# Optimization experiments

Hardware: AMD Instinct MI355X
Metric: run time of the kernel (lower is better)

## Reference

```python
import jax, jax.numpy as jnp
import numpy as np
import math

B, N, K, H = 128, 39, 10, 256
RATIO = 0.8
K1 = math.ceil(RATIO * N)    # 32
K2 = math.ceil(RATIO * K1)   # 26
K3 = math.ceil(RATIO * K2)   # 21


def _edge_conv(x_flat, nb, n, w, b):
    # DynamicEdgeConv: per-graph kNN on features (self included, as torch_cluster.knn),
    # message = relu(Linear([x_i, x_j - x_i])), max aggregation over the K neighbors.
    f = x_flat.shape[-1]
    x = x_flat.reshape(nb, n, f)
    sq = jnp.sum(x * x, axis=-1)                                   # [nb,n]
    d = sq[:, :, None] + sq[:, None, :] - 2.0 * jnp.einsum('bif,bjf->bij', x, x)
    _, idx = jax.lax.top_k(-d, K)                                  # [nb,n,K] nearest
    xj = x[jnp.arange(nb)[:, None, None], idx]                     # [nb,n,K,f]
    xi = x[:, :, None, :]
    msg = jnp.concatenate([jnp.broadcast_to(xi, xj.shape), xj - xi], axis=-1)
    h = jax.nn.relu(msg @ w + b)
    return jnp.max(h, axis=2).reshape(nb * n, -1)


def _gcn_score(x_flat, adj, w, b):
    # GCNConv(in,1) with self-loops + symmetric normalization (SAGPool score layer)
    nb, n, _ = adj.shape
    x = x_flat.reshape(nb, n, -1)
    a = adj + jnp.eye(n, dtype=adj.dtype)
    dinv = jax.lax.rsqrt(jnp.sum(a, axis=-1))
    an = a * dinv[:, :, None] * dinv[:, None, :]
    s = jnp.einsum('bij,bjf->bif', an, x @ w) + b
    return s[..., 0]                                               # [nb,n]


def _sag_pool(x_flat, adj, k, w, b):
    # SAGPool: GCN score, per-graph top-k, gate kept nodes by tanh(score), filter adj.
    nb, n, _ = adj.shape
    score = _gcn_score(x_flat, adj, w, b)
    top, loc = jax.lax.top_k(score, k)                             # [nb,k]
    bi = jnp.arange(nb)[:, None]
    x = x_flat.reshape(nb, n, -1)
    xp = x[bi, loc] * jnp.tanh(top)[..., None]
    adj_p = adj[jnp.arange(nb)[:, None, None], loc[:, :, None], loc[:, None, :]]
    perm = (bi * n + loc).reshape(-1)                              # flat node ids
    return xp.reshape(nb * k, -1), adj_p, perm


def _bn(x, g, b, eps=1e-5):
    m = jnp.mean(x, axis=0)
    v = jnp.var(x, axis=0)
    return (x - m) * jax.lax.rsqrt(v + eps) * g + b


def _readout(x_flat, nb, k):
    x = x_flat.reshape(nb, k, -1)
    return jnp.concatenate([jnp.max(x, axis=1), jnp.mean(x, axis=1)], axis=1)


def reference(x, adj, w_mlp1, b_mlp1, w_mlp2, b_mlp2, w_mlp3, b_mlp3, w_mlp6, b_mlp6,
              bn1_g, bn1_b, bn2_g, bn2_b, bn3_g, bn3_b,
              p1_w, p1_b, p2_w, p2_b, p3_w, p3_b,
              lin1_w, lin1_b, lin2_w, lin2_b, lin3_w, lin3_b,
              lin4_w, lin4_b, lin5_w, lin5_b, lin6_w, lin6_b):
    relu = jax.nn.relu
    deg_gt = jnp.sum(adj, axis=-1).reshape(B * N)                  # degree(edge_index[0])

    def decoder(xf):
        d = jnp.tanh(_edge_conv(xf, B, N, w_mlp3, b_mlp3))         # conv4
        d = jnp.tanh(_edge_conv(d, B, N, w_mlp2, b_mlp2))          # conv5
        return _edge_conv(d, B, N, w_mlp6, b_mlp6)                 # conv6

    def degree_head(xf):
        h = relu(xf @ lin4_w + lin4_b)
        h = relu(h @ lin5_w + lin5_b)
        return relu(h @ lin6_w + lin6_b)

    # ---- level 1 ----
    h1 = relu(_bn(_edge_conv(x.reshape(B * N, N), B, N, w_mlp1, b_mlp1), bn1_g, bn1_b))
    xp1, adj1, perm1 = _sag_pool(h1, adj, K1, p1_w, p1_b)
    x_out1 = jnp.zeros_like(h1).at[perm1].set(xp1)
    x_dec1 = decoder(x_out1)
    x_degree = degree_head(x_out1)   # source reuses this tensor for levels 2/3 preds
    gt1, pred1 = deg_gt[perm1], x_degree[perm1]
    r1 = _readout(xp1, B, K1)

    # ---- level 2 ----
    h2 = relu(_bn(_edge_conv(xp1, B, K1, w_mlp2, b_mlp2), bn2_g, bn2_b))
    xp2, adj2, perm2 = _sag_pool(h2, adj1, K2, p2_w, p2_b)
    inner2 = jnp.zeros_like(h2).at[perm2].set(xp2)
    x_out2 = jnp.zeros_like(h1).at[perm1].set(inner2)
    x_dec2 = decoder(x_out2)
    gt2, pred2 = deg_gt[perm2], x_degree[perm2]
    r2 = _readout(xp2, B, K2)

    # ---- level 3 ----
    h3 = relu(_bn(_edge_conv(xp2, B, K2, w_mlp3, b_mlp3), bn3_g, bn3_b))
    xp3, adj3, perm3 = _sag_pool(h3, adj2, K3, p3_w, p3_b)
    inner3 = jnp.zeros_like(h3).at[perm3].set(xp3)
    x_out3 = jnp.zeros_like(h1).at[perm2].set(inner3)  # faithful: source uses perm_2 here
    x_dec3 = decoder(x_out3)
    gt3, pred3 = deg_gt[perm3], x_degree[perm3]
    r3 = _readout(xp3, B, K3)

    z = r1 + r2 + r3
    z = relu(z @ lin1_w + lin1_b)
    z = relu(z @ lin2_w + lin2_b)
    probs = jax.nn.softmax(z @ lin3_w + lin3_b, axis=1)
    return (probs, x_dec1, x_dec2, x_dec3, gt1, pred1, gt2, pred2, gt3, pred3)


def setup_inputs() -> dict:
    key = jax.random.key(0)
    ks = jax.random.split(key, 32)
    rn = lambda i, shape: jax.random.normal(ks[i], shape, dtype=jnp.float32) * 0.05
    x = jax.random.normal(ks[0], (B, N, N), dtype=jnp.float32)
    adj = (jax.random.uniform(ks[1], (B, N, N)) < 0.2).astype(jnp.float32)
    adj = adj * (1.0 - jnp.eye(N, dtype=jnp.float32))
    return dict(
        x=x, adj=adj,
        w_mlp1=rn(2, (2 * N, H)), b_mlp1=rn(3, (H,)),
        w_mlp2=rn(4, (2 * H, H)), b_mlp2=rn(5, (H,)),
        w_mlp3=rn(6, (2 * H, H)), b_mlp3=rn(7, (H,)),
        w_mlp6=rn(8, (2 * H, N)), b_mlp6=rn(9, (N,)),
        bn1_g=jnp.ones((H,), jnp.float32), bn1_b=jnp.zeros((H,), jnp.float32),
        bn2_g=jnp.ones((H,), jnp.float32), bn2_b=jnp.zeros((H,), jnp.float32),
        bn3_g=jnp.ones((H,), jnp.float32), bn3_b=jnp.zeros((H,), jnp.float32),
        p1_w=rn(10, (H, 1)), p1_b=rn(11, (1,)),
        p2_w=rn(12, (H, 1)), p2_b=rn(13, (1,)),
        p3_w=rn(14, (H, 1)), p3_b=rn(15, (1,)),
        lin1_w=rn(16, (2 * H, H)), lin1_b=rn(17, (H,)),
        lin2_w=rn(18, (H, H // 2)), lin2_b=rn(19, (H // 2,)),
        lin3_w=rn(20, (H // 2, 2)), lin3_b=rn(21, (2,)),
        lin4_w=rn(22, (H, H)), lin4_b=rn(23, (H,)),
        lin5_w=rn(24, (H, H // 2)), lin5_b=rn(25, (H // 2,)),
        lin6_w=rn(26, (H // 2, 1)), lin6_b=rn(27, (1,)))
```

## Files before the change

kernel.cpp:

```cpp
#include <hip/hip_runtime.h>
#include <cmath>

#define B_   128
#define N_   39
#define KNN_ 10
#define H_   256
#define K1_  32
#define K2_  26
#define K3_  21

static inline int cdiv(int a, int b) { return (a + b - 1) / b; }

typedef __attribute__((ext_vector_type(8))) short short8;
typedef __attribute__((ext_vector_type(4))) short short4v;
typedef __attribute__((ext_vector_type(4))) float floatx4;

__device__ inline short f2b(float f) {
  unsigned u = __float_as_uint(f);
  u += 0x7fff + ((u >> 16) & 1);
  return (short)(u >> 16);
}
__device__ inline float b2f(short h) {
  return __uint_as_float(((unsigned)(unsigned short)h) << 16);
}
__device__ inline void f2b3(float v, short& h, short& m, short& l) {
  h = f2b(v);
  float r1 = v - b2f(h);
  m = f2b(r1);
  l = f2b(r1 - b2f(m));
}

__global__ void prep_kernel(
    const float* __restrict__ w1, const float* __restrict__ w2,
    const float* __restrict__ w3, const float* __restrict__ w6,
    const float* __restrict__ l4, const float* __restrict__ l5,
    const float* __restrict__ x, const float* __restrict__ adj,
    short* __restrict__ wt1h, short* __restrict__ wt1m, short* __restrict__ wt1l,
    short* __restrict__ wt2h, short* __restrict__ wt2m, short* __restrict__ wt2l,
    short* __restrict__ wt3h, short* __restrict__ wt3m, short* __restrict__ wt3l,
    short* __restrict__ wt6h, short* __restrict__ wt6m,
    short* __restrict__ l4h, short* __restrict__ l4m,
    short* __restrict__ l5h, short* __restrict__ l5m,
    short* __restrict__ xsph, short* __restrict__ xspm, short* __restrict__ xspl,
    float* __restrict__ deg) {
  int task = blockIdx.y;
  int t = blockIdx.x * 256 + threadIdx.x;
  if (task == 0) {
    if (t >= 512 * 64) return;
    int nn = t >> 6, k = t & 63;
    float v = 0.f;
    if (k < 39) v = (nn < 256) ? w1[k * 256 + nn] - w1[(39 + k) * 256 + nn]
                               : w1[(39 + k) * 256 + (nn - 256)];
    short h, m, l; f2b3(v, h, m, l);
    wt1h[t] = h; wt1m[t] = m; wt1l[t] = l;
  } else if (task == 1) {
    if (t >= 512 * 256) return;
    int nn = t >> 8, k = t & 255;
    float v = (nn < 256) ? w2[k * 256 + nn] - w2[(256 + k) * 256 + nn]
                         : w2[(256 + k) * 256 + (nn - 256)];
    short h, m, l; f2b3(v, h, m, l);
    wt2h[t] = h; wt2m[t] = m; wt2l[t] = l;
  } else if (task == 2) {
    if (t >= 512 * 256) return;
    int nn = t >> 8, k = t & 255;
    float v = (nn < 256) ? w3[k * 256 + nn] - w3[(256 + k) * 256 + nn]
                         : w3[(256 + k) * 256 + (nn - 256)];
    short h, m, l; f2b3(v, h, m, l);
    wt3h[t] = h; wt3m[t] = m; wt3l[t] = l;
  } else if (task == 3) {
    if (t >= 78 * 256) return;
    int nn = t >> 8, k = t & 255;
    float v = (nn < 39) ? w6[k * 39 + nn] - w6[(256 + k) * 39 + nn]
                        : w6[(256 + k) * 39 + (nn - 39)];
    short h, m, l; f2b3(v, h, m, l);
    wt6h[t] = h; wt6m[t] = m;
  } else if (task == 4) {
    if (t >= 256 * 256) return;
    int nn = t >> 8, k = t & 255;
    short h, m, l; f2b3(l4[k * 256 + nn], h, m, l);
    l4h[t] = h; l4m[t] = m;
  } else if (task == 5) {
    if (t >= 128 * 256) return;
    int nn = t >> 8, k = t & 255;
    short h, m, l; f2b3(l5[k * 128 + nn], h, m, l);
    l5h[t] = h; l5m[t] = m;
  } else if (task == 6) {
    if (t >= 4992 * 64) return;
    int r = t >> 6, k = t & 63;
    float v = (k < 39) ? x[r * 39 + k] : 0.f;
    short h, m, l; f2b3(v, h, m, l);
    xsph[t] = h; xspm[t] = m; xspl[t] = l;
  } else {
    if (t >= B_ * N_) return;
    const float* row = adj + (size_t)t * N_;
    float s = 0.f;
    for (int j = 0; j < N_; ++j) s += row[j];
    deg[t] = s;
  }
}

__global__ __launch_bounds__(512) void knn_gemm_kernel(
    const short* __restrict__ kxh, const short* __restrict__ kxm, const short* __restrict__ kxl,
    int knt, int kKs, int kn, int kF32, int* __restrict__ idx, int knnB,
    const short* __restrict__ Ah, const short* __restrict__ Am, const short* __restrict__ Al,
    int gnt, int gK,
    const short* __restrict__ Wh, const short* __restrict__ Wm, const short* __restrict__ Wl,
    float* __restrict__ C0, int gM, int gN, int gyB,
    size_t Astride, size_t Cstride) {
  extern __shared__ char smem[];
  int tid = threadIdx.x;
  int wave = tid >> 6, lane = tid & 63;
  int lm = lane & 15, lk = (lane >> 4) * 8;
  if ((int)blockIdx.x < knnB) {
    short* sh_h = (short*)smem;
    short* sh_m = sh_h + 48 * 40;
    short* sh_l = sh_m + 48 * 40;
    float* Gs   = (float*)(sh_l + 48 * 40);
    float* diag = Gs + 48 * 49;
    int b = blockIdx.x;
    int nt = (kn + 15) >> 4;
    int tasks = nt * nt;
    floatx4 acc[2] = {};
    int stage_elems = 384 * knt;
    for (int k0 = 0; k0 < kF32; k0 += 32) {
      for (int e = tid; e < stage_elems; e += 512) {
        int a = e / 384, rem = e - a * 384;
        int r = rem >> 3, c4 = (rem & 7) * 4;
        const short* src = (a == 0) ? kxh : (a == 1) ? kxm : kxl;
        short* dst = (a == 0) ? sh_h : (a == 1) ? sh_m : sh_l;
        *(short4v*)&dst[r * 40 + c4] =
            *(const short4v*)&src[((size_t)(b * kn + r)) * kKs + k0 + c4];
      }
      __syncthreads();
#pragma unroll
      for (int ai = 0; ai < 2; ++ai) {
        int t = wave + ai * 8;
        if (t < tasks) {
          int ti = t / nt, tj = t - ti * nt;
          int ra = (ti * 16 + lm) * 40 + lk;
          int rb = (tj * 16 + lm) * 40 + lk;
          short8 ah = *(const short8*)&sh_h[ra];
          short8 am = *(const short8*)&sh_m[ra];
          short8 bh = *(const short8*)&sh_h[rb];
          short8 bm = *(const short8*)&sh_m[rb];
          floatx4 a = acc[ai];
          a = __builtin_amdgcn_mfma_f32_16x16x32_bf16(ah, bh, a, 0, 0, 0);
          a = __builtin_amdgcn_mfma_f32_16x16x32_bf16(ah, bm, a, 0, 0, 0);
          a = __builtin_amdgcn_mfma_f32_16x16x32_bf16(am, bh, a, 0, 0, 0);
          if (knt == 3) {
            short8 al = *(const short8*)&sh_l[ra];
            short8 bl = *(const short8*)&sh_l[rb];
            a = __builtin_amdgcn_mfma_f32_16x16x32_bf16(ah, bl, a, 0, 0, 0);
            a = __builtin_amdgcn_mfma_f32_16x16x32_bf16(al, bh, a, 0, 0, 0);
            a = __builtin_amdgcn_mfma_f32_16x16x32_bf16(am, bm, a, 0, 0, 0);
          }
          acc[ai] = a;
        }
      }
      __syncthreads();
    }
#pragma unroll
    for (int ai = 0; ai < 2; ++ai) {
      int t = wave + ai * 8;
      if (t < tasks) {
        int ti = t / nt, tj = t - ti * nt;
        int col = tj * 16 + lm;
        int rbase = ti * 16 + (lane >> 4) * 4;
#pragma unroll
        for (int r = 0; r < 4; ++r) Gs[(rbase + r) * 49 + col] = acc[ai][r];
      }
    }
    __syncthreads();
    if (tid < 48) diag[tid] = (tid < kn) ? Gs[tid * 49 + tid] : INFINITY;
    __syncthreads();
    for (int row = wave; row < kn; row += 8) {
      float gii = diag[row];
      float dj = (lane < kn) ? (gii + diag[lane] - 2.f * Gs[row * 49 + lane]) : INFINITY;
      int rank = 0;
      for (int j = 0; j < kn; ++j) {
        float djp = gii + diag[j] - 2.f * Gs[row * 49 + j];
        rank += (djp < dj || (djp == dj && j < lane)) ? 1 : 0;
      }
      if (lane < kn && rank < KNN_)
        idx[(size_t)(b * kn + row) * KNN_ + rank] = lane;
    }
  } else {
    short* Ash = (short*)smem;
    short* Asm = Ash + 128 * 40;
    short* Asl = Asm + 128 * 40;
    short* Bsh = (short*)smem + gnt * 128 * 40;
    short* Bsm = Bsh + 128 * 40;
    short* Bsl = Bsm + 128 * 40;
    int gb = blockIdx.x - knnB;
    int gxB = (gN + 127) >> 7;
    int gx = gb % gxB;
    int rest = gb / gxB;
    int gy = rest % gyB;
    int gz = rest / gyB;
    const short* A_h = Ah + (size_t)gz * Astride;
    const short* A_m = Am ? Am + (size_t)gz * Astride : nullptr;
    const short* A_l = Al ? Al + (size_t)gz * Astride : nullptr;
    float* C = C0 + (size_t)gz * Cstride;
    int row0 = gy * 128, col0 = gx * 128;
    int wm = wave & 1, wn = wave >> 1;
    floatx4 acc[4][2] = {};
    for (int k0 = 0; k0 < gK; k0 += 32) {
      for (int e = tid; e < gnt * 512; e += 512) {
        int a = e >> 9, rem = e & 511;
        int r = rem >> 2, kc = (rem & 3) * 8;
        const short* src = (a == 0) ? A_h : (a == 1) ? A_m : A_l;
        short* dst = (a == 0) ? Ash : (a == 1) ? Asm : Asl;
        *(short8*)&dst[r * 40 + kc] = *(const short8*)&src[((size_t)(row0 + r)) * gK + k0 + kc];
      }
      for (int e = tid; e < gnt * 512; e += 512) {
        int a = e >> 9, rem = e & 511;
        int r = rem >> 2, kc = (rem & 3) * 8;
        const short* src = (a == 0) ? Wh : (a == 1) ? Wm : Wl;
        short* dst = (a == 0) ? Bsh : (a == 1) ? Bsm : Bsl;
        *(short8*)&dst[r * 40 + kc] = *(const short8*)&src[((size_t)(col0 + r)) * gK + k0 + kc];
      }
      __syncthreads();
      short8 afh[4], afm[4], afl[4];
#pragma unroll
      for (int mi = 0; mi < 4; ++mi) {
        int ro = (wm * 64 + mi * 16 + lm) * 40 + lk;
        afh[mi] = *(const short8*)&Ash[ro];
        if (gnt == 3) {
          afm[mi] = *(const short8*)&Asm[ro];
          afl[mi] = *(const short8*)&Asl[ro];
        } else {
          afm[mi] = *(const short8*)&Asm[ro];
        }
      }
#pragma unroll
      for (int ni = 0; ni < 2; ++ni) {
        int ro = (wn * 32 + ni * 16 + lm) * 40 + lk;
        short8 bfh = *(const short8*)&Bsh[ro];
        short8 bfm = *(const short8*)&Bsm[ro];
#pragma unroll
        for (int mi = 0; mi < 4; ++mi) {
          floatx4 a = acc[mi][ni];
          a = __builtin_amdgcn_mfma_f32_16x16x32_bf16(afh[mi], bfh, a, 0, 0, 0);
          a = __builtin_amdgcn_mfma_f32_16x16x32_bf16(afh[mi], bfm, a, 0, 0, 0);
          a = __builtin_amdgcn_mfma_f32_16x16x32_bf16(afm[mi], bfh, a, 0, 0, 0);
          if (gnt == 3) {
            short8 bfl = *(const short8*)&Bsl[ro];
            a = __builtin_amdgcn_mfma_f32_16x16x32_bf16(afh[mi], bfl, a, 0, 0, 0);
            a = __builtin_amdgcn_mfma_f32_16x16x32_bf16(afl[mi], bfh, a, 0, 0, 0);
            a = __builtin_amdgcn_mfma_f32_16x16x32_bf16(afm[mi], bfm, a, 0, 0, 0);
          }
          acc[mi][ni] = a;
        }
      }
      __syncthreads();
    }
    int lr = (lane >> 4) * 4;
#pragma unroll
    for (int mi = 0; mi < 4; ++mi)
#pragma unroll
      for (int ni = 0; ni < 2; ++ni) {
        int colg = col0 + wn * 32 + ni * 16 + lm;
        if (colg >= gN) continue;
#pragma unroll
        for (int r = 0; r < 4; ++r) {
          int rowg = row0 + wm * 64 + mi * 16 + lr + r;
          C[(size_t)rowg * gN + colg] = acc[mi][ni][r];
        }
      }
  }
}

__global__ __launch_bounds__(256) void degree_head_kernel(
    const short* __restrict__ Xh, const short* __restrict__ Xm,
    const short* __restrict__ W4h, const short* __restrict__ W4m, const float* __restrict__ b4,
    const short* __restrict__ W5h, const short* __restrict__ W5m, const float* __restrict__ b5,
    const float* __restrict__ w6, const float* __restrict__ b6,
    float* __restrict__ xdeg) {
  __shared__ __attribute__((aligned(16))) short Ash[32 * 40];
  __shared__ __attribute__((aligned(16))) short Asm[32 * 40];
  __shared__ __attribute__((aligned(16))) short Bsh[256 * 40];
  __shared__ __attribute__((aligned(16))) short Bsm[256 * 40];
  __shared__ __attribute__((aligned(16))) short H1h[32][264];
  __shared__ __attribute__((aligned(16))) short H1m[32][264];
  __shared__ float rowsum[32];
  int tid = threadIdx.x;
  int wave = tid >> 6, lane = tid & 63;
  int lm = lane & 15, g = lane >> 4, lk = g * 8;
  int row0 = blockIdx.x * 32;

  floatx4 acc[2][4] = {};
  for (int k0 = 0; k0 < 256; k0 += 32) {
    {
      int e = tid;
      int a = e >> 7, rem = e & 127;
      int r = rem >> 2, kc = (rem & 3) * 8;
      const short* src = a ? Xm : Xh;
      short* dst = a ? Asm : Ash;
      *(short8*)&dst[r * 40 + kc] = *(const short8*)&src[(size_t)(row0 + r) * 256 + k0 + kc];
    }
#pragma unroll
    for (int i = 0; i < 8; ++i) {
      int e = tid + i * 256;
      int a = e >> 10, rem = e & 1023;
      int r = rem >> 2, kc = (rem & 3) * 8;
      const short* src = a ? W4m : W4h;
      short* dst = a ? Bsm : Bsh;
      *(short8*)&dst[r * 40 + kc] = *(const short8*)&src[(size_t)r * 256 + k0 + kc];
    }
    __syncthreads();
    short8 afh[2], afm[2];
#pragma unroll
    for (int rt = 0; rt < 2; ++rt) {
      int ro = (rt * 16 + lm) * 40 + lk;
      afh[rt] = *(const short8*)&Ash[ro];
      afm[rt] = *(const short8*)&Asm[ro];
    }
#pragma unroll
    for (int ct = 0; ct < 4; ++ct) {
      int ro = (wave * 64 + ct * 16 + lm) * 40 + lk;
      short8 bfh = *(const short8*)&Bsh[ro];
      short8 bfm = *(const short8*)&Bsm[ro];
#pragma unroll
      for (int rt = 0; rt < 2; ++rt) {
        floatx4 a = acc[rt][ct];
        a = __builtin_amdgcn_mfma_f32_16x16x32_bf16(afh[rt], bfh, a, 0, 0, 0);
        a = __builtin_amdgcn_mfma_f32_16x16x32_bf16(afh[rt], bfm, a, 0, 0, 0);
        a = __builtin_amdgcn_mfma_f32_16x16x32_bf16(afm[rt], bfh, a, 0, 0, 0);
        acc[rt][ct] = a;
      }
    }
    __syncthreads();
  }
#pragma unroll
  for (int rt = 0; rt < 2; ++rt)
#pragma unroll
    for (int ct = 0; ct < 4; ++ct) {
      int col = wave * 64 + ct * 16 + lm;
      float bv = b4[col];
#pragma unroll
      for (int r = 0; r < 4; ++r) {
        int row = rt * 16 + g * 4 + r;
        float v = fmaxf(acc[rt][ct][r] + bv, 0.f);
        short hh = f2b(v);
        H1h[row][col] = hh;
        H1m[row][col] = f2b(v - b2f(hh));
      }
    }
  if (tid < 32) rowsum[tid] = 0.f;
  __syncthreads();

  floatx4 acc2[2][2] = {};
  for (int k0 = 0; k0 < 256; k0 += 32) {
#pragma unroll
    for (int i = 0; i < 4; ++i) {
      int e = tid + i * 256;
      int a = e >> 9, rem = e & 511;
      int r = rem >> 2, kc = (rem & 3) * 8;
      const short* src = a ? W5m : W5h;
      short* dst = a ? Bsm : Bsh;
      *(short8*)&dst[r * 40 + kc] = *(const short8*)&src[(size_t)r * 256 + k0 + kc];
    }
    __syncthreads();
    short8 afh[2], afm[2];
#pragma unroll
    for (int rt = 0; rt < 2; ++rt) {
      afh[rt] = *(const short8*)&H1h[rt * 16 + lm][k0 + lk];
      afm[rt] = *(const short8*)&H1m[rt * 16 + lm][k0 + lk];
    }
#pragma unroll
    for (int ct = 0; ct < 2; ++ct) {
      int ro = (wave * 32 + ct * 16 + lm) * 40 + lk;
      short8 bfh = *(const short8*)&Bsh[ro];
      short8 bfm = *(const short8*)&Bsm[ro];
#pragma unroll
      for (int rt = 0; rt < 2; ++rt) {
        floatx4 a = acc2[rt][ct];
        a = __builtin_amdgcn_mfma_f32_16x16x32_bf16(afh[rt], bfh, a, 0, 0, 0);
        a = __builtin_amdgcn_mfma_f32_16x16x32_bf16(afh[rt], bfm, a, 0, 0, 0);
        a = __builtin_amdgcn_mfma_f32_16x16x32_bf16(afm[rt], bfh, a, 0, 0, 0);
        acc2[rt][ct] = a;
      }
    }
    __syncthreads();
  }

#pragma unroll
  for (int rt = 0; rt < 2; ++rt) {
#pragma unroll
    for (int r = 0; r < 4; ++r) {
      float p = 0.f;
#pragma unroll
      for (int ct = 0; ct < 2; ++ct) {
        int col = wave * 32 + ct * 16 + lm;
        float v = fmaxf(acc2[rt][ct][r] + b5[col], 0.f);
        p += v * w6[col];
      }
#pragma unroll
      for (int off = 1; off < 16; off <<= 1) p += __shfl_xor(p, off, 64);
      if (lm == 0) atomicAdd(&rowsum[rt * 16 + g * 4 + r], p);
    }
  }
  __syncthreads();
  if (tid < 32) xdeg[row0 + tid] = fmaxf(rowsum[tid] + b6[0], 0.f);
}

__global__ __launch_bounds__(256) void rowgemm_kernel(
    const float* __restrict__ A, const float* __restrict__ W, const float* __restrict__ bias,
    float* __restrict__ C, int N, int K, int act) {
  __shared__ float a[512];
  int row = blockIdx.x;
  for (int k = threadIdx.x; k < K; k += 256) a[k] = A[(size_t)row * K + k];
  __syncthreads();
  for (int c = threadIdx.x; c < N; c += 256) {
    float s = 0.f;
    for (int k = 0; k < K; k += 4) {
      float4 av = *(const float4*)&a[k];
      s += av.x * W[(size_t)k * N + c];
      s += av.y * W[(size_t)(k + 1) * N + c];
      s += av.z * W[(size_t)(k + 2) * N + c];
      s += av.w * W[(size_t)(k + 3) * N + c];
    }
    float v = s + (bias ? bias[c] : 0.f);
    if (act == 1) v = fmaxf(v, 0.f);
    C[(size_t)row * N + c] = v;
  }
}

__global__ void wavedot_gemm_kernel(const float* __restrict__ A, const float* __restrict__ W,
                                    const float* __restrict__ bias, float* __restrict__ C,
                                    int M, int N, int K, int act) {
  int wid = (blockIdx.x * blockDim.x + threadIdx.x) >> 6;
  int lane = threadIdx.x & 63;
  if (wid >= M * N) return;
  int row = wid / N, col = wid - row * N;
  const float* ar = A + (size_t)row * K;
  float s = 0.f;
  for (int k = lane; k < K; k += 64) s += ar[k] * W[(size_t)k * N + col];
  for (int off = 32; off; off >>= 1) s += __shfl_down(s, off, 64);
  if (lane == 0) {
    float v = s + (bias ? bias[col] : 0.f);
    if (act == 1) v = fmaxf(v, 0.f);
    C[(size_t)row * N + col] = v;
  }
}

__global__ void edge_agg_kernel(const float* __restrict__ AB, const float* __restrict__ bias,
                                const int* __restrict__ idx, int n, int Hc, int act,
                                int rows, int per,
                                float* __restrict__ out,
                                short* __restrict__ outh, short* __restrict__ outm,
                                short* __restrict__ outl) {
  int t = blockIdx.x * blockDim.x + threadIdx.x;
  if (t >= rows * Hc) return;
  int r = t / Hc, h = t - r * Hc;
  int d = r / per, rloc = r - d * per;
  int b = rloc / n;
  int s2 = 2 * Hc;
  float av = AB[(size_t)r * s2 + h] + bias[h];
  const int* ir = idx + ((size_t)d * per + rloc) * KNN_;
  int base = d * per + b * n;
  float m = -INFINITY;
  for (int k = 0; k < KNN_; ++k) {
    float v = av + AB[(size_t)(base + ir[k]) * s2 + Hc + h];
    v = fmaxf(v, 0.f);
    m = fmaxf(m, v);
  }
  if (act == 2) m = tanhf(m);
  if (out) out[t] = m;
  if (outh) {
    short hh, mm, ll;
    f2b3(m, hh, mm, ll);
    outh[t] = hh; outm[t] = mm;
    if (outl) outl[t] = ll;
  }
}

__global__ void bn_stats_kernel(const float* __restrict__ xx, int M,
                                const float* __restrict__ g, const float* __restrict__ bb,
                                float* __restrict__ scsh) {
  int c = blockIdx.x;
  double s = 0.0, s2 = 0.0;
  for (int r = threadIdx.x; r < M; r += 256) {
    double v = (double)xx[(size_t)r * H_ + c];
    s += v; s2 += v * v;
  }
  __shared__ double sh[256], sh2[256];
  sh[threadIdx.x] = s; sh2[threadIdx.x] = s2;
  __syncthreads();
  for (int o = 128; o; o >>= 1) {
    if (threadIdx.x < o) { sh[threadIdx.x] += sh[threadIdx.x + o]; sh2[threadIdx.x] += sh2[threadIdx.x + o]; }
    __syncthreads();
  }
  if (threadIdx.x == 0) {
    double mean = sh[0] / M;
    double var = sh2[0] / M - mean * mean;
    float rstd = 1.f / sqrtf((float)var + 1e-5f);
    float sc = rstd * g[c];
    scsh[c] = sc;
    scsh[H_ + c] = bb[c] - (float)mean * sc;
  }
}

__global__ void bnrowdot_kernel(const float* __restrict__ t1, const float* __restrict__ scsh,
                                const float* __restrict__ pw, int M, float* __restrict__ ys) {
  int wid = (blockIdx.x * blockDim.x + threadIdx.x) >> 6;
  int lane = threadIdx.x & 63;
  if (wid >= M) return;
  const float* xr = t1 + (size_t)wid * H_;
  float s = 0.f;
  for (int k = lane; k < H_; k += 64) {
    float v = fmaxf(xr[k] * scsh[k] + scsh[H_ + k], 0.f);
    s += v * pw[k];
  }
  for (int off = 32; off; off >>= 1) s += __shfl_down(s, off, 64);
  if (lane == 0) ys[wid] = s;
}

__global__ __launch_bounds__(256) void sag_select_kernel(
    const float* __restrict__ ysg,
    const float* __restrict__ adj_in, int n, int k,
    const float* __restrict__ pb,
    int* __restrict__ perm, float* __restrict__ tantg, int* __restrict__ locsg,
    float* __restrict__ adjp,
    const float* __restrict__ deg, const float* __restrict__ xdeg,
    float* __restrict__ gt, float* __restrict__ pred) {
  __shared__ float ys[40], dinv[40], scs[40];
  __shared__ int locs[40];
  int b = blockIdx.x;
  int i = threadIdx.x;
  if (i < n) {
    ys[i] = ysg[b * n + i];
    const float* ar = adj_in + ((size_t)b * n + i) * n;
    float sum = 1.f;
    for (int j = 0; j < n; ++j) sum += ar[j];
    dinv[i] = 1.f / sqrtf(sum);
  }
  __syncthreads();
  if (i < n) {
    const float* ar = adj_in + ((size_t)b * n + i) * n;
    float acc = 0.f;
    for (int j = 0; j < n; ++j) {
      float a = ar[j] + (i == j ? 1.f : 0.f);
      acc += a * dinv[j] * ys[j];
    }
    scs[i] = dinv[i] * acc + pb[0];
  }
  __syncthreads();
  if (i < n) {
    float si = scs[i];
    int rank = 0;
    for (int j = 0; j < n; ++j) {
      float sj = scs[j];
      rank += (sj > si || (sj == si && j < i)) ? 1 : 0;
    }
    if (rank < k) {
      tantg[b * k + rank] = tanhf(si);
      locsg[b * k + rank] = i;
      locs[rank] = i;
      perm[b * k + rank] = b * n + i;
    }
  }
  __syncthreads();
  if (adjp) {
    for (int e = threadIdx.x; e < k * k; e += 256) {
      int t1i = e / k, t2i = e - t1i * k;
      adjp[(size_t)b * k * k + e] = adj_in[((size_t)b * n + locs[t1i]) * n + locs[t2i]];
    }
  }
  if (gt && threadIdx.x < k) {
    int p = b * n + locs[threadIdx.x];
    gt[b * k + threadIdx.x] = deg[p];
    pred[b * k + threadIdx.x] = xdeg[p];
  }
}

__global__ void pool_scatter_kernel(
    const float* __restrict__ t1, const float* __restrict__ scsh,
    const float* __restrict__ tantg, const int* __restrict__ locsg,
    const int* __restrict__ remap, int n, int k,
    short* __restrict__ xph, short* __restrict__ xpm, short* __restrict__ xpl,
    short* __restrict__ soh, short* __restrict__ som) {
  int t = blockIdx.x * blockDim.x + threadIdx.x;
  if (t >= B_ * k * H_) return;
  int r = t >> 8, hc = t & 255;
  int b = r / k, rr = r - b * k;
  int own = b * n + locsg[b * k + rr];
  float v = fmaxf(t1[(size_t)own * H_ + hc] * scsh[hc] + scsh[H_ + hc], 0.f) * tantg[b * k + rr];
  short hh, mm, ll;
  f2b3(v, hh, mm, ll);
  xph[t] = hh; xpm[t] = mm; xpl[t] = ll;
  int tgt = remap ? remap[own] : own;
  size_t so = (size_t)tgt * H_ + hc;
  soh[so] = hh; som[so] = mm;
}

__global__ void readout_kernel(const short* __restrict__ xph, const short* __restrict__ xpm,
                               const short* __restrict__ xpl, int k, int accum,
                               float* __restrict__ z) {
  int t = blockIdx.x * blockDim.x + threadIdx.x;
  if (t >= B_ * H_) return;
  int b = t >> 8, hc = t & 255;
  float mx = -INFINITY, sm = 0.f;
  for (int r = 0; r < k; ++r) {
    size_t o = ((size_t)(b * k + r)) * H_ + hc;
    float v = b2f(xph[o]) + b2f(xpm[o]) + b2f(xpl[o]);
    mx = fmaxf(mx, v);
    sm += v;
  }
  float* zb = z + (size_t)b * 2 * H_;
  float mean = sm / (float)k;
  if (accum) { zb[hc] += mx; zb[H_ + hc] += mean; }
  else       { zb[hc] = mx;  zb[H_ + hc] = mean; }
}

__global__ void gtpred_kernel(const float* __restrict__ deg, const float* __restrict__ xdeg,
                              const int* __restrict__ perm, int M,
                              float* __restrict__ gt, float* __restrict__ pred) {
  int t = blockIdx.x * blockDim.x + threadIdx.x;
  if (t >= M) return;
  int p = perm[t];
  gt[t] = deg[p];
  pred[t] = xdeg[p];
}

__global__ void softmax2_kernel(const float* __restrict__ logits, float* __restrict__ probs) {
  int b = blockIdx.x * blockDim.x + threadIdx.x;
  if (b >= B_) return;
  float a = logits[2 * b], c = logits[2 * b + 1];
  float m = fmaxf(a, c);
  float ea = expf(a - m), ec = expf(c - m);
  float inv = 1.f / (ea + ec);
  probs[2 * b] = ea * inv;
  probs[2 * b + 1] = ec * inv;
}

extern "C" void kernel_launch(void* const* d_in, const int* in_sizes, int n_in,
                              void* d_out, int out_size, void* d_ws, size_t ws_size,
                              hipStream_t stream) {
  auto in = [&](int i) { return (const float*)d_in[i]; };
  const float* x      = in(0);
  const float* adj    = in(1);
  const float* w_mlp1 = in(2);  const float* b_mlp1 = in(3);
  const float* w_mlp2 = in(4);  const float* b_mlp2 = in(5);
  const float* w_mlp3 = in(6);  const float* b_mlp3 = in(7);
  const float* w_mlp6 = in(8);  const float* b_mlp6 = in(9);
  const float* bn1_g = in(10);  const float* bn1_b = in(11);
  const float* bn2_g = in(12);  const float* bn2_b = in(13);
  const float* bn3_g = in(14);  const float* bn3_b = in(15);
  const float* p1_w = in(16);   const float* p1_b = in(17);
  const float* p2_w = in(18);   const float* p2_b = in(19);
  const float* p3_w = in(20);   const float* p3_b = in(21);
  const float* lin1_w = in(22); const float* lin1_b = in(23);
  const float* lin2_w = in(24); const float* lin2_b = in(25);
  const float* lin3_w = in(26); const float* lin3_b = in(27);
  const float* lin4_w = in(28); const float* lin4_b = in(29);
  const float* lin5_w = in(30); const float* lin5_b = in(31);
  const float* lin6_w = in(32); const float* lin6_b = in(33);

  float* out = (float*)d_out;
  float* out_probs = out;
  float* out_dec1  = out_probs + 256;
  float* out_gt1   = out_dec1 + 3 * 4992 * 39;
  float* out_pred1 = out_gt1 + 4096;
  float* out_gt2   = out_pred1 + 4096;
  float* out_pred2 = out_gt2 + 3328;
  float* out_gt3   = out_pred2 + 3328;
  float* out_pred3 = out_gt3 + 2688;

  char* base = (char*)d_ws;
  size_t off = 0;
  auto allocf = [&](size_t n) -> float* {
    float* p = (float*)(base + off);
    off += ((n * sizeof(float) + 255) & ~(size_t)255);
    return p;
  };
  auto alloci = [&](size_t n) -> int* {
    int* p = (int*)(base + off);
    off += ((n * sizeof(int) + 255) & ~(size_t)255);
    return p;
  };
  auto allocs = [&](size_t n) -> short* {
    short* p = (short*)(base + off);
    off += ((n * sizeof(short) + 255) & ~(size_t)255);
    return p;
  };

  const size_t S = (size_t)4992 * 256;
  const size_t AB_S = (size_t)4992 * 512;
  const int SI = 4992 * KNN_;

  short* wt1h = allocs(512 * 64); short* wt1m = allocs(512 * 64); short* wt1l = allocs(512 * 64);
  short* wt2h = allocs(512 * 256); short* wt2m = allocs(512 * 256); short* wt2l = allocs(512 * 256);
  short* wt3h = allocs(512 * 256); short* wt3m = allocs(512 * 256); short* wt3l = allocs(512 * 256);
  short* wt6h = allocs(78 * 256);  short* wt6m = allocs(78 * 256);
  short* l4h = allocs(256 * 256);  short* l4m = allocs(256 * 256);
  short* l5h = allocs(128 * 256);  short* l5m = allocs(128 * 256);
  short* xsph = allocs(4992 * 64); short* xspm = allocs(4992 * 64); short* xspl = allocs(4992 * 64);
  float* deg  = allocf(4992);
  float* xdeg = allocf(4992);
  float* ysg  = allocf(4992);
  int* idxb = alloci(3 * SI);
  float* AB3 = allocf(3 * AB_S);
  float* trunk_t1 = allocf(S);
  float* scsh = allocf(512);
  float* tantg = allocf(4096);
  int* locsg = alloci(4096);
  short* xph = allocs((size_t)4096 * 256); short* xpm = allocs((size_t)4096 * 256); short* xpl = allocs((size_t)4096 * 256);
  size_t ms0 = off;
  short* xoutb_h = allocs(3 * S);
  short* xoutb_m = allocs(3 * S);
  size_t msz = off - ms0;
  short* t1b_h = allocs(3 * S);
  short* t1b_m = allocs(3 * S);
  float* adj1 = allocf(128 * 32 * 32);
  float* adj2 = allocf(128 * 26 * 26);
  int* perm1 = alloci(4096); int* perm2 = alloci(3328); int* perm3 = alloci(2688);
  float* z  = allocf(128 * 512);
  float* z1 = allocf(128 * 256);
  float* z2 = allocf(128 * 128);
  float* logits = allocf(256);
  if (off > ws_size) return;

  short* t2b_h = xoutb_h; short* t2b_m = xoutb_m;

  const size_t LDS3 = 6 * 128 * 40 * sizeof(short);
  const size_t LDS2 = 4 * 128 * 40 * sizeof(short);

  prep_kernel<<<dim3(1248, 8), 256, 0, stream>>>(
      w_mlp1, w_mlp2, w_mlp3, w_mlp6, lin4_w, lin5_w, x, adj,
      wt1h, wt1m, wt1l, wt2h, wt2m, wt2l, wt3h, wt3m, wt3l, wt6h, wt6m,
      l4h, l4m, l5h, l5m, xsph, xspm, xspl, deg);
  hipMemsetAsync(xoutb_h, 0, msz, stream);

  knn_gemm_kernel<<<B_ + 4 * 39, 512, LDS3, stream>>>(
      xsph, xspm, xspl, 3, 64, N_, 64, idxb, B_,
      xsph, xspm, xspl, 3, 64, wt1h, wt1m, wt1l, AB3, 4992, 512, 39, 0, 0);
  edge_agg_kernel<<<cdiv(4992 * 256, 256), 256, 0, stream>>>(AB3, b_mlp1, idxb, N_, 256, 0, 4992, 4992,
                                                             trunk_t1, nullptr, nullptr, nullptr);
  bn_stats_kernel<<<H_, 256, 0, stream>>>(trunk_t1, 4992, bn1_g, bn1_b, scsh);
  bnrowdot_kernel<<<cdiv(4992 * 64, 256), 256, 0, stream>>>(trunk_t1, scsh, p1_w, 4992, ysg);
  sag_select_kernel<<<B_, 256, 0, stream>>>(ysg, adj, N_, K1_, p1_b,
                                            perm1, tantg, locsg, adj1,
                                            nullptr, nullptr, nullptr, nullptr);
  pool_scatter_kernel<<<cdiv(B_ * K1_ * H_, 256), 256, 0, stream>>>(
      trunk_t1, scsh, tantg, locsg, nullptr, N_, K1_, xph, xpm, xpl, xoutb_h, xoutb_m);
  readout_kernel<<<cdiv(B_ * H_, 256), 256, 0, stream>>>(xph, xpm, xpl, K1_, 0, z);
  degree_head_kernel<<<156, 256, 0, stream>>>(
      xoutb_h, xoutb_m, l4h, l4m, lin4_b, l5h, l5m, lin5_b, lin6_w, lin6_b, xdeg);
  gtpred_kernel<<<cdiv(4096, 256), 256, 0, stream>>>(deg, xdeg, perm1, 4096, out_gt1, out_pred1);

  knn_gemm_kernel<<<B_ + 4 * 32, 512, LDS3, stream>>>(
      xph, xpm, xpl, 3, 256, K1_, 256, idxb, B_,
      xph, xpm, xpl, 3, 256, wt2h, wt2m, wt2l, AB3, 4096, 512, 32, 0, 0);
  edge_agg_kernel<<<cdiv(4096 * 256, 256), 256, 0, stream>>>(AB3, b_mlp2, idxb, K1_, 256, 0, 4096, 4096,
                                                             trunk_t1, nullptr, nullptr, nullptr);
  bn_stats_kernel<<<H_, 256, 0, stream>>>(trunk_t1, 4096, bn2_g, bn2_b, scsh);
  bnrowdot_kernel<<<cdiv(4096 * 64, 256), 256, 0, stream>>>(trunk_t1, scsh, p2_w, 4096, ysg);
  sag_select_kernel<<<B_, 256, 0, stream>>>(ysg, adj1, K1_, K2_, p2_b,
                                            perm2, tantg, locsg, adj2,
                                            deg, xdeg, out_gt2, out_pred2);
  pool_scatter_kernel<<<cdiv(B_ * K2_ * H_, 256), 256, 0, stream>>>(
      trunk_t1, scsh, tantg, locsg, perm1, K1_, K2_, xph, xpm, xpl, xoutb_h + S, xoutb_m + S);
  readout_kernel<<<cdiv(B_ * H_, 256), 256, 0, stream>>>(xph, xpm, xpl, K2_, 1, z);

  knn_gemm_kernel<<<B_ + 4 * 26, 512, LDS3, stream>>>(
      xph, xpm, xpl, 3, 256, K2_, 256, idxb, B_,
      xph, xpm, xpl, 3, 256, wt3h, wt3m, wt3l, AB3, 3328, 512, 26, 0, 0);
  edge_agg_kernel<<<cdiv(3328 * 256, 256), 256, 0, stream>>>(AB3, b_mlp3, idxb, K2_, 256, 0, 3328, 3328,
                                                             trunk_t1, nullptr, nullptr, nullptr);
  bn_stats_kernel<<<H_, 256, 0, stream>>>(trunk_t1, 3328, bn3_g, bn3_b, scsh);
  bnrowdot_kernel<<<cdiv(3328 * 64, 256), 256, 0, stream>>>(trunk_t1, scsh, p3_w, 3328, ysg);
  sag_select_kernel<<<B_, 256, 0, stream>>>(ysg, adj2, K2_, K3_, p3_b,
                                            perm3, tantg, locsg, nullptr,
                                            deg, xdeg, out_gt3, out_pred3);
  pool_scatter_kernel<<<cdiv(B_ * K3_ * H_, 256), 256, 0, stream>>>(
      trunk_t1, scsh, tantg, locsg, perm2, K2_, K3_, xph, xpm, xpl, xoutb_h + 2 * S, xoutb_m + 2 * S);
  readout_kernel<<<cdiv(B_ * H_, 256), 256, 0, stream>>>(xph, xpm, xpl, K3_, 1, z);

  rowgemm_kernel<<<128, 256, 0, stream>>>(z, lin1_w, lin1_b, z1, 256, 512, 1);
  rowgemm_kernel<<<128, 256, 0, stream>>>(z1, lin2_w, lin2_b, z2, 128, 256, 1);
  wavedot_gemm_kernel<<<cdiv(128 * 2 * 64, 256), 256, 0, stream>>>(z2, lin3_w, lin3_b, logits, 128, 2, 128, 0);
  softmax2_kernel<<<1, 128, 0, stream>>>(logits, out_probs);

  knn_gemm_kernel<<<3 * B_ + 4 * 39 * 3, 512, LDS2, stream>>>(
      xoutb_h, xoutb_m, nullptr, 2, 256, N_, 256, idxb, 3 * B_,
      xoutb_h, xoutb_m, nullptr, 2, 256, wt3h, wt3m, nullptr, AB3, 4992, 512, 39, S, AB_S);
  edge_agg_kernel<<<cdiv(3 * 4992 * 256, 256), 256, 0, stream>>>(
      AB3, b_mlp3, idxb, N_, 256, 2, 3 * 4992, 4992, nullptr, t1b_h, t1b_m, nullptr);
  knn_gemm_kernel<<<3 * B_ + 4 * 39 * 3, 512, LDS2, stream>>>(
      t1b_h, t1b_m, nullptr, 2, 256, N_, 256, idxb, 3 * B_,
      t1b_h, t1b_m, nullptr, 2, 256, wt2h, wt2m, nullptr, AB3, 4992, 512, 39, S, AB_S);
  edge_agg_kernel<<<cdiv(3 * 4992 * 256, 256), 256, 0, stream>>>(
      AB3, b_mlp2, idxb, N_, 256, 2, 3 * 4992, 4992, nullptr, t2b_h, t2b_m, nullptr);
  knn_gemm_kernel<<<3 * B_ + 1 * 39 * 3, 512, LDS2, stream>>>(
      t2b_h, t2b_m, nullptr, 2, 256, N_, 256, idxb, 3 * B_,
      t2b_h, t2b_m, nullptr, 2, 256, wt6h, wt6m, nullptr, AB3, 4992, 78, 39, S, (size_t)4992 * 78);
  edge_agg_kernel<<<cdiv(3 * 4992 * 39, 256), 256, 0, stream>>>(
      AB3, b_mlp6, idxb, N_, 39, 0, 3 * 4992, 4992, out_dec1, nullptr, nullptr, nullptr);
}
```

Measured before the change: 521.8 us.

## Fuse decoder kNN, edge GEMM and max-aggregation into one per-graph kernel

Replaces the three decoder stages, each a knn_gemm launch plus an edge_agg launch, with a single dec_stage_kernel per stage. Each block handles one graph: it computes the Gram matrix with split-bf16 MFMA, ranks neighbours in LDS, runs the 512-column edge GEMM with weights streamed through LDS, and applies the bias, relu, max and tanh epilogue in place. This removes the AB3 intermediate round trip through global memory and halves the launch count. The trade-off is 384 blocks using about 128KB of LDS each, which allows only one block per CU and leaves low occupancy, plus weight reloads per graph.

```diff
diff --git a/kernel.cpp b/kernel.cpp
--- a/kernel.cpp
+++ b/kernel.cpp
@@ -270,6 +270,190 @@
   }
 }
 
+__global__ __launch_bounds__(512) void dec_stage_kernel(
+    const short* __restrict__ Xh, const short* __restrict__ Xm,
+    const short* __restrict__ Wh, const short* __restrict__ Wm,
+    const float* __restrict__ bias, int gN, int mode,
+    short* __restrict__ Oh, short* __restrict__ Om, float* __restrict__ Ofp) {
+  extern __shared__ char smem[];
+  short* A_h = (short*)smem;
+  short* A_m = A_h + 48 * 264;
+  short* W_h = A_m + 48 * 264;
+  short* W_m = W_h + 128 * 72;
+  float* Gre  = (float*)(W_m + 128 * 72);
+  int*   idxl = (int*)(Gre + 10140);
+  float* sBias = (float*)(idxl + 480);
+  int tid = threadIdx.x;
+  int wave = tid >> 6, lane = tid & 63;
+  int lm = lane & 15, lg = lane >> 4, lk = lg * 8;
+  size_t rowbase = (size_t)blockIdx.x * 39;
+
+  for (int e = tid; e < 48 * 32 * 2; e += 512) {
+    int a = e >= 48 * 32;
+    int rem = a ? e - 48 * 32 : e;
+    int r = rem >> 5, c8 = (rem & 31) * 8;
+    short8 v = {};
+    if (r < 39) v = *(const short8*)&(a ? Xm : Xh)[(rowbase + r) * 256 + c8];
+    *(short8*)&(a ? A_m : A_h)[r * 264 + c8] = v;
+  }
+  {
+    int nb = mode ? 39 : 256;
+    for (int e = tid; e < nb; e += 512) sBias[e] = bias[e];
+  }
+  __syncthreads();
+
+  {
+    float* G = Gre;
+    float* diag = G + 48 * 49;
+    floatx4 gacc[2] = {};
+    for (int k0 = 0; k0 < 256; k0 += 32) {
+#pragma unroll
+      for (int ai = 0; ai < 2; ++ai) {
+        int t = wave + ai * 8;
+        if (t < 9) {
+          int ti = t / 3, tj = t - ti * 3;
+          int ra = (ti * 16 + lm) * 264 + k0 + lk;
+          int rb = (tj * 16 + lm) * 264 + k0 + lk;
+          short8 ah = *(const short8*)&A_h[ra];
+          short8 am = *(const short8*)&A_m[ra];
+          short8 bh = *(const short8*)&A_h[rb];
+          short8 bm = *(const short8*)&A_m[rb];
+          floatx4 a = gacc[ai];
+          a = __builtin_amdgcn_mfma_f32_16x16x32_bf16(ah, bh, a, 0, 0, 0);
+          a = __builtin_amdgcn_mfma_f32_16x16x32_bf16(ah, bm, a, 0, 0, 0);
+          a = __builtin_amdgcn_mfma_f32_16x16x32_bf16(am, bh, a, 0, 0, 0);
+          gacc[ai] = a;
+        }
+      }
+    }
+#pragma unroll
+    for (int ai = 0; ai < 2; ++ai) {
+      int t = wave + ai * 8;
+      if (t < 9) {
+        int ti = t / 3, tj = t - ti * 3;
+        int col = tj * 16 + lm;
+        int rb2 = ti * 16 + lg * 4;
+#pragma unroll
+        for (int r = 0; r < 4; ++r) G[(rb2 + r) * 49 + col] = gacc[ai][r];
+      }
+    }
+    __syncthreads();
+    if (tid < 48) diag[tid] = (tid < 39) ? G[tid * 49 + tid] : INFINITY;
+    __syncthreads();
+    for (int row = wave; row < 39; row += 8) {
+      float gii = diag[row];
+      float dj = (lane < 39) ? (gii + diag[lane] - 2.f * G[row * 49 + lane]) : INFINITY;
+      int rank = 0;
+      for (int j = 0; j < 39; ++j) {
+        float djp = gii + diag[j] - 2.f * G[row * 49 + j];
+        rank += (djp < dj || (djp == dj && j < lane)) ? 1 : 0;
+      }
+      if (lane < 39 && rank < KNN_) idxl[row * KNN_ + rank] = lane;
+    }
+  }
+
+  floatx4 acc[4][3] = {};
+#pragma unroll
+  for (int nc = 0; nc < 4; ++nc) {
+    if (nc * 128 >= gN) continue;
+    int cols = gN - nc * 128; if (cols > 128) cols = 128;
+    for (int kc = 0; kc < 256; kc += 64) {
+      for (int e = tid; e < 2048; e += 512) {
+        int a = e >= 1024;
+        int rem = a ? e - 1024 : e;
+        int r = rem >> 3, c8 = (rem & 7) * 8;
+        short8 v = {};
+        if (r < cols) v = *(const short8*)&(a ? Wm : Wh)[(size_t)(nc * 128 + r) * 256 + kc + c8];
+        *(short8*)&(a ? W_m : W_h)[r * 72 + c8] = v;
+      }
+      __syncthreads();
+      if (wave * 16 < cols) {
+#pragma unroll
+        for (int ks = 0; ks < 2; ++ks) {
+          int k0 = kc + ks * 32;
+          int rw = (wave * 16 + lm) * 72 + ks * 32 + lk;
+          short8 bh = *(const short8*)&W_h[rw];
+          short8 bm = *(const short8*)&W_m[rw];
+#pragma unroll
+          for (int mt = 0; mt < 3; ++mt) {
+            int ra = (mt * 16 + lm) * 264 + k0 + lk;
+            short8 ah = *(const short8*)&A_h[ra];
+            short8 am = *(const short8*)&A_m[ra];
+            floatx4 a = acc[nc][mt];
+            a = __builtin_amdgcn_mfma_f32_16x16x32_bf16(ah, bh, a, 0, 0, 0);
+            a = __builtin_amdgcn_mfma_f32_16x16x32_bf16(ah, bm, a, 0, 0, 0);
+            a = __builtin_amdgcn_mfma_f32_16x16x32_bf16(am, bh, a, 0, 0, 0);
+            acc[nc][mt] = a;
+          }
+        }
+      }
+      __syncthreads();
+    }
+  }
+
+  if (mode == 0) {
+    float* GsB = Gre;
+#pragma unroll
+    for (int nc = 2; nc < 4; ++nc)
+#pragma unroll
+      for (int mt = 0; mt < 3; ++mt)
+#pragma unroll
+        for (int r = 0; r < 4; ++r) {
+          int row = mt * 16 + lg * 4 + r;
+          if (row < 39) GsB[row * 260 + (nc - 2) * 128 + wave * 16 + lm] = acc[nc][mt][r];
+        }
+    __syncthreads();
+#pragma unroll
+    for (int nc = 0; nc < 2; ++nc)
+#pragma unroll
+      for (int mt = 0; mt < 3; ++mt)
+#pragma unroll
+        for (int r = 0; r < 4; ++r) {
+          int row = mt * 16 + lg * 4 + r;
+          if (row >= 39) continue;
+          int col = nc * 128 + wave * 16 + lm;
+          float av = acc[nc][mt][r] + sBias[col];
+          float mx = -INFINITY;
+#pragma unroll
+          for (int k = 0; k < KNN_; ++k) {
+            int nb = idxl[row * KNN_ + k];
+            float v = fmaxf(av + GsB[nb * 260 + col], 0.f);
+            mx = fmaxf(mx, v);
+          }
+          mx = tanhf(mx);
+          short hh = f2b(mx);
+          short mm = f2b(mx - b2f(hh));
+          size_t o = (rowbase + row) * 256 + col;
+          Oh[o] = hh; Om[o] = mm;
+        }
+  } else {
+    float* Gs = Gre;
+    if (wave * 16 < 78) {
+#pragma unroll
+      for (int mt = 0; mt < 3; ++mt)
+#pragma unroll
+        for (int r = 0; r < 4; ++r) {
+          int row = mt * 16 + lg * 4 + r;
+          int col = wave * 16 + lm;
+          if (row < 39 && col < 78) Gs[row * 80 + col] = acc[0][mt][r];
+        }
+    }
+    __syncthreads();
+    for (int e = tid; e < 39 * 39; e += 512) {
+      int row = e / 39, h = e - row * 39;
+      float av = Gs[row * 80 + h] + sBias[h];
+      float mx = -INFINITY;
+#pragma unroll
+      for (int k = 0; k < KNN_; ++k) {
+        int nb = idxl[row * KNN_ + k];
+        float v = fmaxf(av + Gs[nb * 80 + 39 + h], 0.f);
+        mx = fmaxf(mx, v);
+      }
+      Ofp[(rowbase + row) * 39 + h] = mx;
+    }
+  }
+}
+
 __global__ __launch_bounds__(256) void degree_head_kernel(
     const short* __restrict__ Xh, const short* __restrict__ Xm,
     const short* __restrict__ W4h, const short* __restrict__ W4m, const float* __restrict__ b4,
@@ -724,7 +908,13 @@
   short* t2b_h = xoutb_h; short* t2b_m = xoutb_m;
 
   const size_t LDS3 = 6 * 128 * 40 * sizeof(short);
-  const size_t LDS2 = 4 * 128 * 40 * sizeof(short);
+  const size_t DEC_LDS = 131056;
+  static int dec_lds_set = 0;
+  if (!dec_lds_set) {
+    hipFuncSetAttribute(reinterpret_cast<const void*>(dec_stage_kernel),
+                        hipFuncAttributeMaxDynamicSharedMemorySize, (int)DEC_LDS);
+    dec_lds_set = 1;
+  }
 
   prep_kernel<<<dim3(1248, 8), 256, 0, stream>>>(
       w_mlp1, w_mlp2, w_mlp3, w_mlp6, lin4_w, lin5_w, x, adj,
@@ -782,19 +972,10 @@
   wavedot_gemm_kernel<<<cdiv(128 * 2 * 64, 256), 256, 0, stream>>>(z2, lin3_w, lin3_b, logits, 128, 2, 128, 0);
   softmax2_kernel<<<1, 128, 0, stream>>>(logits, out_probs);
 
-  knn_gemm_kernel<<<3 * B_ + 4 * 39 * 3, 512, LDS2, stream>>>(
-      xoutb_h, xoutb_m, nullptr, 2, 256, N_, 256, idxb, 3 * B_,
-      xoutb_h, xoutb_m, nullptr, 2, 256, wt3h, wt3m, nullptr, AB3, 4992, 512, 39, S, AB_S);
-  edge_agg_kernel<<<cdiv(3 * 4992 * 256, 256), 256, 0, stream>>>(
-      AB3, b_mlp3, idxb, N_, 256, 2, 3 * 4992, 4992, nullptr, t1b_h, t1b_m, nullptr);
-  knn_gemm_kernel<<<3 * B_ + 4 * 39 * 3, 512, LDS2, stream>>>(
-      t1b_h, t1b_m, nullptr, 2, 256, N_, 256, idxb, 3 * B_,
-      t1b_h, t1b_m, nullptr, 2, 256, wt2h, wt2m, nullptr, AB3, 4992, 512, 39, S, AB_S);
-  edge_agg_kernel<<<cdiv(3 * 4992 * 256, 256), 256, 0, stream>>>(
-      AB3, b_mlp2, idxb, N_, 256, 2, 3 * 4992, 4992, nullptr, t2b_h, t2b_m, nullptr);
-  knn_gemm_kernel<<<3 * B_ + 1 * 39 * 3, 512, LDS2, stream>>>(
-      t2b_h, t2b_m, nullptr, 2, 256, N_, 256, idxb, 3 * B_,
-      t2b_h, t2b_m, nullptr, 2, 256, wt6h, wt6m, nullptr, AB3, 4992, 78, 39, S, (size_t)4992 * 78);
-  edge_agg_kernel<<<cdiv(3 * 4992 * 39, 256), 256, 0, stream>>>(
-      AB3, b_mlp6, idxb, N_, 39, 0, 3 * 4992, 4992, out_dec1, nullptr, nullptr, nullptr);
-}
+  dec_stage_kernel<<<3 * B_, 512, DEC_LDS, stream>>>(
+      xoutb_h, xoutb_m, wt3h, wt3m, b_mlp3, 512, 0, t1b_h, t1b_m, nullptr);
+  dec_stage_kernel<<<3 * B_, 512, DEC_LDS, stream>>>(
+      t1b_h, t1b_m, wt2h, wt2m, b_mlp2, 512, 0, t2b_h, t2b_m, nullptr);
+  dec_stage_kernel<<<3 * B_, 512, DEC_LDS, stream>>>(
+      t2b_h, t2b_m, wt6h, wt6m, b_mlp6, 78, 1, nullptr, nullptr, out_dec1);
+}
```

Result: slower. 621.6 us (+19.1%).

## Fuse decoder edge-conv GEMM with neighbor max-aggregation in one kernel

Applied to the files above, without the earlier changes.

Adds a kernel that computes the per-node A/B projections for three graphs (117 rows) in a block, keeps the results in LDS, and does the kNN max aggregation, with tanh and bf16 split, in place. This replaces the separate GEMM part of the knn_gemm launch and the edge_agg kernel in the three decoder edge-conv layers, so the AB intermediate no longer goes through global memory. The knn kernel is now launched only for the kNN blocks with a smaller LDS size. The cost is a large LDS footprint per block (about 70 KB) and only 512 or 128 blocks, which limits occupancy.

```diff
diff --git a/kernel.cpp b/kernel.cpp
--- a/kernel.cpp
+++ b/kernel.cpp
@@ -270,6 +270,125 @@
   }
 }
 
+__global__ __launch_bounds__(512) void dec_gemmagg_kernel(
+    const short* __restrict__ Xh, const short* __restrict__ Xm,
+    const short* __restrict__ Wh, const short* __restrict__ Wm,
+    const float* __restrict__ bias, int nA,
+    const int* __restrict__ idxg, int mode,
+    short* __restrict__ Oh, short* __restrict__ Om, float* __restrict__ Ofp) {
+  extern __shared__ char smem[];
+  short* Ash = (short*)smem;
+  short* Asm = Ash + 128 * 40;
+  short* Bsh = Asm + 128 * 40;
+  short* Bsm = Bsh + 128 * 40;
+  float* Cs  = (float*)smem;
+  int*   idxl = (int*)(smem + 66560);
+  int tid = threadIdx.x;
+  int wave = tid >> 6, lane = tid & 63;
+  int lm = lane & 15, lg = lane >> 4, lk = lg * 8;
+  int gx = blockIdx.x, gy = blockIdx.y;
+  int col0 = gx * 128;
+  int row0g = gy * 117;
+  int wm = wave & 1, wn = wave >> 1;
+
+  for (int e = tid; e < 117 * KNN_; e += 512)
+    idxl[e] = idxg[(size_t)(row0g + e / KNN_) * KNN_ + (e % KNN_)];
+
+  floatx4 acc[4][2] = {};
+  for (int k0 = 0; k0 < 256; k0 += 32) {
+    for (int e = tid; e < 1024; e += 512) {
+      int a = e >> 9, rem = e & 511;
+      int r = rem >> 2, kc = (rem & 3) * 8;
+      short8 v = {};
+      if (r < 117) v = *(const short8*)&(a ? Xm : Xh)[(size_t)(row0g + r) * 256 + k0 + kc];
+      *(short8*)&(a ? Asm : Ash)[r * 40 + kc] = v;
+    }
+    for (int e = tid; e < 1024; e += 512) {
+      int a = e >> 9, rem = e & 511;
+      int r = rem >> 2, kc = (rem & 3) * 8;
+      int p = col0 + r;
+      short8 v = {};
+      if (p < 2 * nA) {
+        int wr = (p >> 1) + (p & 1) * nA;
+        v = *(const short8*)&(a ? Wm : Wh)[(size_t)wr * 256 + k0 + kc];
+      }
+      *(short8*)&(a ? Bsm : Bsh)[r * 40 + kc] = v;
+    }
+    __syncthreads();
+    short8 afh[4], afm[4];
+#pragma unroll
+    for (int mi = 0; mi < 4; ++mi) {
+      int ro = (wm * 64 + mi * 16 + lm) * 40 + lk;
+      afh[mi] = *(const short8*)&Ash[ro];
+      afm[mi] = *(const short8*)&Asm[ro];
+    }
+#pragma unroll
+    for (int ni = 0; ni < 2; ++ni) {
+      int ro = (wn * 32 + ni * 16 + lm) * 40 + lk;
+      short8 bfh = *(const short8*)&Bsh[ro];
+      short8 bfm = *(const short8*)&Bsm[ro];
+#pragma unroll
+      for (int mi = 0; mi < 4; ++mi) {
+        floatx4 a = acc[mi][ni];
+        a = __builtin_amdgcn_mfma_f32_16x16x32_bf16(afh[mi], bfh, a, 0, 0, 0);
+        a = __builtin_amdgcn_mfma_f32_16x16x32_bf16(afh[mi], bfm, a, 0, 0, 0);
+        a = __builtin_amdgcn_mfma_f32_16x16x32_bf16(afm[mi], bfh, a, 0, 0, 0);
+        acc[mi][ni] = a;
+      }
+    }
+    __syncthreads();
+  }
+  int lr = lg * 4;
+#pragma unroll
+  for (int mi = 0; mi < 4; ++mi)
+#pragma unroll
+    for (int ni = 0; ni < 2; ++ni) {
+      int col = wn * 32 + ni * 16 + lm;
+#pragma unroll
+      for (int r = 0; r < 4; ++r) {
+        int row = wm * 64 + mi * 16 + lr + r;
+        Cs[row * 130 + col] = acc[mi][ni][r];
+      }
+    }
+  __syncthreads();
+  if (mode == 0) {
+    for (int e = tid; e < 117 * 64; e += 512) {
+      int r = e >> 6, h = e & 63;
+      int hg = gx * 64 + h;
+      float av = Cs[r * 130 + 2 * h] + bias[hg];
+      const int* ir = &idxl[r * KNN_];
+      int gb = (r / 39) * 39;
+      float mx = -INFINITY;
+#pragma unroll
+      for (int k = 0; k < KNN_; ++k) {
+        int nb = gb + ir[k];
+        float v = fmaxf(av + Cs[nb * 130 + 2 * h + 1], 0.f);
+        mx = fmaxf(mx, v);
+      }
+      mx = tanhf(mx);
+      short hh = f2b(mx);
+      short mm = f2b(mx - b2f(hh));
+      size_t o = (size_t)(row0g + r) * 256 + hg;
+      Oh[o] = hh; Om[o] = mm;
+    }
+  } else {
+    for (int e = tid; e < 117 * 39; e += 512) {
+      int r = e / 39, h = e - r * 39;
+      float av = Cs[r * 130 + 2 * h] + bias[h];
+      const int* ir = &idxl[r * KNN_];
+      int gb = (r / 39) * 39;
+      float mx = -INFINITY;
+#pragma unroll
+      for (int k = 0; k < KNN_; ++k) {
+        int nb = gb + ir[k];
+        float v = fmaxf(av + Cs[nb * 130 + 2 * h + 1], 0.f);
+        mx = fmaxf(mx, v);
+      }
+      Ofp[(size_t)(row0g + r) * 39 + h] = mx;
+    }
+  }
+}
+
 __global__ __launch_bounds__(256) void degree_head_kernel(
     const short* __restrict__ Xh, const short* __restrict__ Xm,
     const short* __restrict__ W4h, const short* __restrict__ W4m, const float* __restrict__ b4,
@@ -724,7 +843,14 @@
   short* t2b_h = xoutb_h; short* t2b_m = xoutb_m;
 
   const size_t LDS3 = 6 * 128 * 40 * sizeof(short);
-  const size_t LDS2 = 4 * 128 * 40 * sizeof(short);
+  const size_t LDSK = 21120;
+  const size_t DECG_LDS = 66560 + 1170 * 4;
+  static int decg_set = 0;
+  if (!decg_set) {
+    hipFuncSetAttribute(reinterpret_cast<const void*>(dec_gemmagg_kernel),
+                        hipFuncAttributeMaxDynamicSharedMemorySize, (int)DECG_LDS);
+    decg_set = 1;
+  }
 
   prep_kernel<<<dim3(1248, 8), 256, 0, stream>>>(
       w_mlp1, w_mlp2, w_mlp3, w_mlp6, lin4_w, lin5_w, x, adj,
@@ -782,19 +908,19 @@
   wavedot_gemm_kernel<<<cdiv(128 * 2 * 64, 256), 256, 0, stream>>>(z2, lin3_w, lin3_b, logits, 128, 2, 128, 0);
   softmax2_kernel<<<1, 128, 0, stream>>>(logits, out_probs);
 
-  knn_gemm_kernel<<<3 * B_ + 4 * 39 * 3, 512, LDS2, stream>>>(
+  knn_gemm_kernel<<<3 * B_, 512, LDSK, stream>>>(
       xoutb_h, xoutb_m, nullptr, 2, 256, N_, 256, idxb, 3 * B_,
-      xoutb_h, xoutb_m, nullptr, 2, 256, wt3h, wt3m, nullptr, AB3, 4992, 512, 39, S, AB_S);
-  edge_agg_kernel<<<cdiv(3 * 4992 * 256, 256), 256, 0, stream>>>(
-      AB3, b_mlp3, idxb, N_, 256, 2, 3 * 4992, 4992, nullptr, t1b_h, t1b_m, nullptr);
-  knn_gemm_kernel<<<3 * B_ + 4 * 39 * 3, 512, LDS2, stream>>>(
+      nullptr, nullptr, nullptr, 2, 256, nullptr, nullptr, nullptr, AB3, 0, 512, 1, 0, 0);
+  dec_gemmagg_kernel<<<dim3(4, 128), 512, DECG_LDS, stream>>>(
+      xoutb_h, xoutb_m, wt3h, wt3m, b_mlp3, 256, idxb, 0, t1b_h, t1b_m, nullptr);
+  knn_gemm_kernel<<<3 * B_, 512, LDSK, stream>>>(
       t1b_h, t1b_m, nullptr, 2, 256, N_, 256, idxb, 3 * B_,
-      t1b_h, t1b_m, nullptr, 2, 256, wt2h, wt2m, nullptr, AB3, 4992, 512, 39, S, AB_S);
-  edge_agg_kernel<<<cdiv(3 * 4992 * 256, 256), 256, 0, stream>>>(
-      AB3, b_mlp2, idxb, N_, 256, 2, 3 * 4992, 4992, nullptr, t2b_h, t2b_m, nullptr);
-  knn_gemm_kernel<<<3 * B_ + 1 * 39 * 3, 512, LDS2, stream>>>(
+      nullptr, nullptr, nullptr, 2, 256, nullptr, nullptr, nullptr, AB3, 0, 512, 1, 0, 0);
+  dec_gemmagg_kernel<<<dim3(4, 128), 512, DECG_LDS, stream>>>(
+      t1b_h, t1b_m, wt2h, wt2m, b_mlp2, 256, idxb, 0, t2b_h, t2b_m, nullptr);
+  knn_gemm_kernel<<<3 * B_, 512, LDSK, stream>>>(
       t2b_h, t2b_m, nullptr, 2, 256, N_, 256, idxb, 3 * B_,
-      t2b_h, t2b_m, nullptr, 2, 256, wt6h, wt6m, nullptr, AB3, 4992, 78, 39, S, (size_t)4992 * 78);
-  edge_agg_kernel<<<cdiv(3 * 4992 * 39, 256), 256, 0, stream>>>(
-      AB3, b_mlp6, idxb, N_, 39, 0, 3 * 4992, 4992, out_dec1, nullptr, nullptr, nullptr);
-}
+      nullptr, nullptr, nullptr, 2, 256, nullptr, nullptr, nullptr, AB3, 0, 512, 1, 0, 0);
+  dec_gemmagg_kernel<<<dim3(1, 128), 512, DECG_LDS, stream>>>(
+      t2b_h, t2b_m, wt6h, wt6m, b_mlp6, 39, idxb, 1, nullptr, nullptr, out_dec1);
+}
```

Result: no change. 526.8 us (+1.0%).
